# Performance work log

Hardware: AMD Instinct MI355X
Metric: run time of the kernel (lower is better)

Reference implementation:

```python
import jax, jax.numpy as jnp
import numpy as np

N = 50000
E = 1600000
IN_CH = 34
HID = 64
OUT = 64
NEG_SLOPE = 0.2


def _gat_layer(x, src, dst, W, a_src, a_dst, bias, heads, out_ch, concat):
    n = x.shape[0]
    xw = (x @ W).reshape(n, heads, out_ch)                      # [N,H,C]
    al_src = jnp.sum(xw * a_src[None], axis=-1)                  # [N,H]
    al_dst = jnp.sum(xw * a_dst[None], axis=-1)                  # [N,H]
    e = jax.nn.leaky_relu(al_src[src] + al_dst[dst], NEG_SLOPE)  # [E,H]
    # segment softmax over incoming edges of each dst node (self-loops ensure non-empty)
    m = jax.ops.segment_max(e, dst, num_segments=n)              # [N,H]
    ex = jnp.exp(e - m[dst])
    denom = jax.ops.segment_sum(ex, dst, num_segments=n)         # [N,H]
    alpha = ex / denom[dst]                                      # [E,H]
    msg = xw[src] * alpha[:, :, None]                            # [E,H,C]
    out = jax.ops.segment_sum(msg, dst, num_segments=n)          # [N,H,C]
    if concat:
        out = out.reshape(n, heads * out_ch)
    else:
        out = out.mean(axis=1)
    return out + bias


def setup_inputs() -> dict:
    key = jax.random.key(0)
    ks = jax.random.split(key, 12)
    x = jax.random.normal(ks[0], (N, IN_CH), dtype=jnp.float32)
    edge_index = jax.random.randint(ks[1], (2, E), 0, N, dtype=jnp.int64)
    # layer 1: heads=2, concat -> 128
    W1 = jax.random.normal(ks[2], (IN_CH, 2 * HID), dtype=jnp.float32) * 0.1
    a_src1 = jax.random.normal(ks[3], (2, HID), dtype=jnp.float32) * 0.1
    a_dst1 = jax.random.normal(ks[4], (2, HID), dtype=jnp.float32) * 0.1
    b1 = jnp.zeros((2 * HID,), dtype=jnp.float32)
    # layer 2: heads=1, mean
    W2 = jax.random.normal(ks[5], (2 * HID, OUT), dtype=jnp.float32) * 0.1
    a_src2 = jax.random.normal(ks[6], (1, OUT), dtype=jnp.float32) * 0.1
    a_dst2 = jax.random.normal(ks[7], (1, OUT), dtype=jnp.float32) * 0.1
    b2 = jnp.zeros((OUT,), dtype=jnp.float32)
    return {"x": x, "edge_index": edge_index, "W1": W1, "a_src1": a_src1,
            "a_dst1": a_dst1, "b1": b1, "W2": W2, "a_src2": a_src2,
            "a_dst2": a_dst2, "b2": b2}


def reference(x, edge_index, W1, a_src1, a_dst1, b1, W2, a_src2, a_dst2, b2):
    n = x.shape[0]
    loops = jnp.arange(n, dtype=edge_index.dtype)
    src = jnp.concatenate([edge_index[0], loops])  # PyG GATConv add_self_loops=True
    dst = jnp.concatenate([edge_index[1], loops])
    h = _gat_layer(x, src, dst, W1, a_src1, a_dst1, b1, heads=2, out_ch=HID, concat=True)
    h = jax.nn.relu(h)
    out = _gat_layer(h, src, dst, W2, a_src2, a_dst2, b2, heads=1, out_ch=OUT, concat=False)
    return out
```

## Files before the change

kernel.cpp:

```cpp
#include <hip/hip_runtime.h>
#include <math.h>

#define N_NODES 50000
#define E_EDGES 1600000
#define IN_CH   34
#define NEG     0.2f
#define NB      196
#define CAP     10000

typedef __attribute__((ext_vector_type(2))) float fv2;

static __device__ __forceinline__ unsigned short f2bf(float f) {
    unsigned int u = __float_as_uint(f);
    u += 0x7fffu + ((u >> 16) & 1u);
    return (unsigned short)(u >> 16);
}
static __device__ __forceinline__ float bflo(unsigned int u) {
    return __uint_as_float(u << 16);
}
static __device__ __forceinline__ float bfhi(unsigned int u) {
    return __uint_as_float(u & 0xffff0000u);
}
static __device__ __forceinline__ float lrelu_exp(float e) {
    return expf(e > 0.f ? e : NEG * e);
}

static __device__ __forceinline__ int scan256_excl(int v, int* wsum) {
    const int lane = threadIdx.x & 63, wv = threadIdx.x >> 6;
    int x = v;
    #pragma unroll
    for (int off = 1; off < 64; off <<= 1) {
        int y = __shfl_up(x, off);
        if (lane >= off) x += y;
    }
    if (lane == 63) wsum[wv] = x;
    __syncthreads();
    if (threadIdx.x < 4) {
        int s = wsum[threadIdx.x];
        #pragma unroll
        for (int off = 1; off < 4; off <<= 1) {
            int y = __shfl_up(s, off);
            if ((int)threadIdx.x >= off) s += y;
        }
        wsum[threadIdx.x] = s;
    }
    __syncthreads();
    const int woff = wv ? wsum[wv - 1] : 0;
    return woff + x - v;
}

__global__ __launch_bounds__(256) void k_bin_node1(
    const int* __restrict__ srcA, const int* __restrict__ dstA,
    int* __restrict__ gcur, unsigned int* __restrict__ binned,
    const float* __restrict__ x, const float* __restrict__ W1,
    const float* __restrict__ a_src, const float* __restrict__ a_dst,
    unsigned short* __restrict__ xw1b,
    float* __restrict__ al_s, float* __restrict__ al_d)
{
    __shared__ __align__(16) char sm[69664];
    const int tid = threadIdx.x;

    if (blockIdx.x < NB) {
        unsigned int* raw  = (unsigned int*)sm;
        unsigned int* ebuf = (unsigned int*)(sm + 32768);
        int* cnt  = (int*)(sm + 65536);
        int* loff = (int*)(sm + 66560);
        int* lcur = (int*)(sm + 67584);
        int* cur  = (int*)(sm + 68608);
        int* wsum = (int*)(sm + 69632);
        cnt[tid] = 0;
        __syncthreads();
        const int base = blockIdx.x * 8192;
        #pragma unroll
        for (int i = 0; i < 32; ++i) {
            const int e = base + i * 256 + tid;
            if (e < E_EDGES) {
                const int d = dstA[e], s = srcA[e];
                raw[i * 256 + tid] = ((unsigned int)d << 16) | (unsigned int)s;
                atomicAdd(&cnt[d >> 8], 1);
            }
        }
        __syncthreads();
        const int v = cnt[tid];
        const int excl = scan256_excl(v, wsum);
        loff[tid] = excl;
        lcur[tid] = excl;
        cur[tid] = (tid < NB && v > 0) ? (tid * CAP + atomicAdd(&gcur[tid], v)) : 0;
        __syncthreads();
        const int mE = min(8192, E_EDGES - base);
        #pragma unroll
        for (int i = 0; i < 32; ++i) {
            const int p = i * 256 + tid;
            if (p < mE) {
                const unsigned int u = raw[p];
                const int q = atomicAdd(&lcur[u >> 24], 1);
                ebuf[q] = u;
            }
        }
        __syncthreads();
        #pragma unroll
        for (int i = 0; i < 32; ++i) {
            const int p = i * 256 + tid;
            if (p < mE) {
                const unsigned int u = ebuf[p];
                const int b = (int)(u >> 24);
                binned[cur[b] + (p - loff[b])] = u;
            }
        }
    } else {
        float* sW  = (float*)sm;
        float* sx  = (float*)(sm + 17952);
        float* sas = (float*)(sm + 22432);
        float* sad = (float*)(sm + 22944);
        for (int i = tid; i < IN_CH * 128; i += 256) {
            int k = i >> 7, c = i & 127;
            sW[k * 132 + c] = W1[i];
        }
        if (tid < 128) { sas[tid] = a_src[tid]; sad[tid] = a_dst[tid]; }
        const int n0 = (blockIdx.x - NB) * 32;
        for (int i = tid; i < 32 * IN_CH; i += 256) {
            int n = i / IN_CH;
            sx[n * 35 + (i - n * IN_CH)] = (n0 + n < N_NODES) ? x[n0 * IN_CH + i] : 0.f;
        }
        __syncthreads();

        const int tc = tid & 31, tn = tid >> 5;
        float acc[4][4] = {{0.f}};
        for (int k = 0; k < IN_CH; ++k) {
            const float4 wv = *reinterpret_cast<const float4*>(&sW[k * 132 + 4 * tc]);
            #pragma unroll
            for (int j = 0; j < 4; ++j) {
                const float hj = sx[(4 * tn + j) * 35 + k];
                acc[j][0] += hj * wv.x; acc[j][1] += hj * wv.y;
                acc[j][2] += hj * wv.z; acc[j][3] += hj * wv.w;
            }
        }
        #pragma unroll
        for (int j = 0; j < 4; ++j) {
            const int node = n0 + 4 * tn + j;
            float ps = 0.f, pd = 0.f;
            #pragma unroll
            for (int c = 0; c < 4; ++c) {
                ps += acc[j][c] * sas[4 * tc + c];
                pd += acc[j][c] * sad[4 * tc + c];
            }
            #pragma unroll
            for (int off = 1; off < 16; off <<= 1) {
                ps += __shfl_xor(ps, off);
                pd += __shfl_xor(pd, off);
            }
            if (node < N_NODES) {
                if ((tc & 15) == 0) {
                    int h = tc >> 4;
                    al_s[node * 2 + h] = ps;
                    al_d[node * 2 + h] = pd;
                }
                ushort4 u;
                u.x = f2bf(acc[j][0]); u.y = f2bf(acc[j][1]);
                u.z = f2bf(acc[j][2]); u.w = f2bf(acc[j][3]);
                *reinterpret_cast<ushort4*>(&xw1b[node * 128 + 4 * tc]) = u;
            }
        }
    }
}

__global__ __launch_bounds__(256) void k_fine(
    const int* __restrict__ gcur, const unsigned int* __restrict__ binned,
    int2* __restrict__ rowspan, int* __restrict__ sorted_src)
{
    __shared__ unsigned int sbin[CAP];
    __shared__ int cnt[256], lcur[256];
    __shared__ int wsum[4];
    const int tid = threadIdx.x;
    const int b = blockIdx.x;
    const int bbase = b * CAP;
    const int cntb = gcur[b];
    cnt[tid] = 0;
    __syncthreads();
    for (int p = tid; p < cntb; p += 256) {
        const unsigned int u = binned[bbase + p];
        sbin[p] = u;
        atomicAdd(&cnt[(u >> 16) & 255], 1);
    }
    __syncthreads();
    const int v = cnt[tid];
    const int excl = scan256_excl(v, wsum);
    const int node = b * 256 + tid;
    if (node < N_NODES) rowspan[node] = make_int2(bbase + excl, bbase + excl + v);
    lcur[tid] = excl;
    __syncthreads();
    for (int p = tid; p < cntb; p += 256) {
        const unsigned int u = sbin[p];
        const int q = atomicAdd(&lcur[(u >> 16) & 255], 1);
        sorted_src[bbase + q] = (int)(u & 0xffffu);
    }
}

__global__ __launch_bounds__(256) void k_gather1(
    const int2* __restrict__ rowspan, const int* __restrict__ sorted_src,
    const unsigned int* __restrict__ xw1u,
    const float* __restrict__ al_s, const float* __restrict__ al_d,
    const float* __restrict__ b1, float* __restrict__ hbuf)
{
    __shared__ float4 AB[2][4][32];
    const int wave = threadIdx.x >> 6;
    const int lane = threadIdx.x & 63;
    const int node = (blockIdx.x * 256 + threadIdx.x) >> 6;
    if (node >= N_NODES) return;
    const int2 span = rowspan[node];
    const int head = lane >> 5;

    const float2 ald  = *reinterpret_cast<const float2*>(&al_d[node * 2]);
    const float2 als0 = *reinterpret_cast<const float2*>(&al_s[node * 2]);
    const float w0h0 = lrelu_exp(als0.x + ald.x);
    const float w0h1 = lrelu_exp(als0.y + ald.y);
    const float wself = head ? w0h1 : w0h0;

    const unsigned int su = xw1u[node * 64 + lane];
    fv2 accX = { wself * bflo(su), wself * bfhi(su) };
    fv2 accY = { 0.f, 0.f };
    float dv0 = 0.f, dv1 = 0.f;
    const float4* ABh = AB[head][wave];

    for (int base = span.x; base < span.y; base += 64) {
        const int rem = span.y - base;
        const int m = rem < 64 ? rem : 64;
        const int mp = (m + 1) & ~1;
        if (lane < m) {
            const int s = sorted_src[base + lane];
            const float2 als = *reinterpret_cast<const float2*>(&al_s[s * 2]);
            const float w0 = lrelu_exp(als.x + ald.x);
            const float w1 = lrelu_exp(als.y + ald.y);
            dv0 += w0; dv1 += w1;
            const float offf = __int_as_float(s << 6);
            ((float2*)&AB[0][wave][lane >> 1])[lane & 1] = make_float2(offf, w0);
            ((float2*)&AB[1][wave][lane >> 1])[lane & 1] = make_float2(offf, w1);
        } else if (lane < mp) {
            const float offf = __int_as_float(node << 6);
            ((float2*)&AB[0][wave][lane >> 1])[lane & 1] = make_float2(offf, 0.f);
            ((float2*)&AB[1][wave][lane >> 1])[lane & 1] = make_float2(offf, 0.f);
        }
        const int P = mp >> 1;
        int p = 0;
        for (; p + 4 <= P; p += 4) {
            const float4 q0 = ABh[p + 0];
            const float4 q1 = ABh[p + 1];
            const float4 q2 = ABh[p + 2];
            const float4 q3 = ABh[p + 3];
            const unsigned int a0 = xw1u[__float_as_int(q0.x) + lane];
            const unsigned int b0 = xw1u[__float_as_int(q0.z) + lane];
            const unsigned int a1 = xw1u[__float_as_int(q1.x) + lane];
            const unsigned int b1v = xw1u[__float_as_int(q1.z) + lane];
            const unsigned int a2 = xw1u[__float_as_int(q2.x) + lane];
            const unsigned int b2 = xw1u[__float_as_int(q2.z) + lane];
            const unsigned int a3 = xw1u[__float_as_int(q3.x) + lane];
            const unsigned int b3 = xw1u[__float_as_int(q3.z) + lane];
            fv2 f;
            f.x = bflo(a0); f.y = bfhi(a0); accX += f * q0.y;
            f.x = bflo(b0); f.y = bfhi(b0); accY += f * q0.w;
            f.x = bflo(a1); f.y = bfhi(a1); accX += f * q1.y;
            f.x = bflo(b1v); f.y = bfhi(b1v); accY += f * q1.w;
            f.x = bflo(a2); f.y = bfhi(a2); accX += f * q2.y;
            f.x = bflo(b2); f.y = bfhi(b2); accY += f * q2.w;
            f.x = bflo(a3); f.y = bfhi(a3); accX += f * q3.y;
            f.x = bflo(b3); f.y = bfhi(b3); accY += f * q3.w;
        }
        for (; p < P; ++p) {
            const float4 q = ABh[p];
            const unsigned int a = xw1u[__float_as_int(q.x) + lane];
            const unsigned int b = xw1u[__float_as_int(q.z) + lane];
            fv2 f;
            f.x = bflo(a); f.y = bfhi(a); accX += f * q.y;
            f.x = bflo(b); f.y = bfhi(b); accY += f * q.w;
        }
    }
    accX += accY;
    #pragma unroll
    for (int off = 32; off; off >>= 1) {
        dv0 += __shfl_xor(dv0, off);
        dv1 += __shfl_xor(dv1, off);
    }
    const float den = head ? (dv1 + w0h1) : (dv0 + w0h0);
    const float2 bv = *reinterpret_cast<const float2*>(&b1[2 * lane]);
    float o0 = accX.x / den + bv.x;
    float o1 = accX.y / den + bv.y;
    o0 = o0 > 0.f ? o0 : 0.f;
    o1 = o1 > 0.f ? o1 : 0.f;
    *reinterpret_cast<float2*>(&hbuf[node * 128 + 2 * lane]) = make_float2(o0, o1);
}

__global__ __launch_bounds__(256) void k_node2(
    const float* __restrict__ hbuf, const float* __restrict__ W2,
    const float* __restrict__ a_src, const float* __restrict__ a_dst,
    unsigned short* __restrict__ xw2b, float* __restrict__ al_s, float* __restrict__ al_d)
{
    __shared__ float sW[128 * 64];
    __shared__ float sh[64 * 129];
    __shared__ float sas[64], sad[64];
    const int tid = threadIdx.x;
    for (int i = tid; i < 128 * 64; i += 256) sW[i] = W2[i];
    if (tid < 64) { sas[tid] = a_src[tid]; sad[tid] = a_dst[tid]; }
    const int n0 = blockIdx.x * 64;
    for (int i = tid; i < 64 * 128; i += 256) {
        int n = i >> 7, c = i & 127;
        sh[n * 129 + c] = (n0 + n < N_NODES) ? hbuf[(long)(n0 + n) * 128 + c] : 0.f;
    }
    __syncthreads();

    const int tc = tid & 15, tn = tid >> 4;
    float acc[4][4] = {{0.f}};
    for (int k = 0; k < 128; ++k) {
        const float4 wv = *reinterpret_cast<const float4*>(&sW[k * 64 + 4 * tc]);
        #pragma unroll
        for (int j = 0; j < 4; ++j) {
            const float hj = sh[(4 * tn + j) * 129 + k];
            acc[j][0] += hj * wv.x; acc[j][1] += hj * wv.y;
            acc[j][2] += hj * wv.z; acc[j][3] += hj * wv.w;
        }
    }
    #pragma unroll
    for (int j = 0; j < 4; ++j) {
        const int node = n0 + 4 * tn + j;
        float ps = 0.f, pd = 0.f;
        #pragma unroll
        for (int c = 0; c < 4; ++c) {
            ps += acc[j][c] * sas[4 * tc + c];
            pd += acc[j][c] * sad[4 * tc + c];
        }
        #pragma unroll
        for (int off = 1; off < 16; off <<= 1) {
            ps += __shfl_xor(ps, off);
            pd += __shfl_xor(pd, off);
        }
        if (node < N_NODES) {
            if (tc == 0) { al_s[node] = ps; al_d[node] = pd; }
            ushort4 u;
            u.x = f2bf(acc[j][0]); u.y = f2bf(acc[j][1]);
            u.z = f2bf(acc[j][2]); u.w = f2bf(acc[j][3]);
            *reinterpret_cast<ushort4*>(&xw2b[node * 64 + 4 * tc]) = u;
        }
    }
}

__global__ __launch_bounds__(256) void k_gather2(
    const int2* __restrict__ rowspan, const int* __restrict__ sorted_src,
    const unsigned int* __restrict__ xw2u,
    const float* __restrict__ al_s, const float* __restrict__ al_d,
    const float* __restrict__ b2, float* __restrict__ out)
{
    __shared__ float4 AB[4][32];
    const int wave = threadIdx.x >> 6;
    const int lane = threadIdx.x & 63;
    const int node = (blockIdx.x * 256 + threadIdx.x) >> 6;
    if (node >= N_NODES) return;
    const int2 span = rowspan[node];
    const int li = lane & 31, hsel = lane >> 5;

    const float ald = al_d[node];
    const float w0s = lrelu_exp(al_s[node] + ald);
    const unsigned int su = xw2u[node * 32 + li];
    const float wself = hsel ? 0.f : w0s;
    fv2 acc = { wself * bflo(su), wself * bfhi(su) };
    float dv = 0.f;
    const float4* ABw = AB[wave];

    for (int base = span.x; base < span.y; base += 64) {
        const int rem = span.y - base;
        const int m = rem < 64 ? rem : 64;
        const int mp = (m + 3) & ~3;
        if (lane < m) {
            const int s = sorted_src[base + lane];
            const float w = lrelu_exp(al_s[s] + ald);
            dv += w;
            ((float2*)&AB[wave][lane >> 1])[lane & 1] =
                make_float2(__int_as_float(s << 5), w);
        } else if (lane < mp) {
            ((float2*)&AB[wave][lane >> 1])[lane & 1] =
                make_float2(__int_as_float(node << 5), 0.f);
        }
        const int P = mp >> 1;
        int p = hsel;
        for (; p + 2 < P; p += 4) {
            const float4 qA = ABw[p];
            const float4 qB = ABw[p + 2];
            const unsigned int aA = xw2u[__float_as_int(qA.x) + li];
            const unsigned int bA = xw2u[__float_as_int(qA.z) + li];
            const unsigned int aB = xw2u[__float_as_int(qB.x) + li];
            const unsigned int bB = xw2u[__float_as_int(qB.z) + li];
            fv2 f;
            f.x = bflo(aA); f.y = bfhi(aA); acc += f * qA.y;
            f.x = bflo(bA); f.y = bfhi(bA); acc += f * qA.w;
            f.x = bflo(aB); f.y = bfhi(aB); acc += f * qB.y;
            f.x = bflo(bB); f.y = bfhi(bB); acc += f * qB.w;
        }
        for (; p < P; p += 2) {
            const float4 q = ABw[p];
            const unsigned int a = xw2u[__float_as_int(q.x) + li];
            const unsigned int b = xw2u[__float_as_int(q.z) + li];
            fv2 f;
            f.x = bflo(a); f.y = bfhi(a); acc += f * q.y;
            f.x = bflo(b); f.y = bfhi(b); acc += f * q.w;
        }
    }
    acc.x += __shfl_xor(acc.x, 32);
    acc.y += __shfl_xor(acc.y, 32);
    #pragma unroll
    for (int off = 32; off; off >>= 1) dv += __shfl_xor(dv, off);
    if (lane < 32) {
        const float den = dv + w0s;
        const float2 bv = *reinterpret_cast<const float2*>(&b2[2 * li]);
        *reinterpret_cast<float2*>(&out[node * 64 + 2 * li]) =
            make_float2(acc.x / den + bv.x, acc.y / den + bv.y);
    }
}

extern "C" void kernel_launch(void* const* d_in, const int* in_sizes, int n_in,
                              void* d_out, int out_size, void* d_ws, size_t ws_size,
                              hipStream_t stream)
{
    const float* x   = (const float*)d_in[0];
    const int*   ei  = (const int*)d_in[1];
    const float* W1  = (const float*)d_in[2];
    const float* as1 = (const float*)d_in[3];
    const float* ad1 = (const float*)d_in[4];
    const float* b1  = (const float*)d_in[5];
    const float* W2  = (const float*)d_in[6];
    const float* as2 = (const float*)d_in[7];
    const float* ad2 = (const float*)d_in[8];
    const float* b2  = (const float*)d_in[9];
    float* out = (float*)d_out;

    const int* srcA = ei;
    const int* dstA = ei + E_EDGES;

    char* ws = (char*)d_ws;
    int2*  rowspan    = (int2*)(ws);
    int*   sorted_src = (int*)(ws + 409600);
    int*   gcur       = (int*)(ws + 8249600);
    float* al_s1      = (float*)(ws + 8251648);
    float* al_d1      = (float*)(ws + 8651648);
    float* al_s2      = (float*)(ws + 9051648);
    float* al_d2      = (float*)(ws + 9251648);
    unsigned short* xw1b = (unsigned short*)(ws + 9451648);
    float* hbuf       = (float*)(ws + 22251648);
    unsigned int* binned = (unsigned int*)hbuf;
    unsigned short* xw2b = (unsigned short*)(ws + 47851648);

    hipMemsetAsync(gcur, 0, NB * sizeof(int), stream);
    hipLaunchKernelGGL(k_bin_node1, dim3(NB + (N_NODES + 31) / 32), dim3(256), 0, stream,
                       srcA, dstA, gcur, binned,
                       x, W1, as1, ad1, xw1b, al_s1, al_d1);
    hipLaunchKernelGGL(k_fine, dim3(NB), dim3(256), 0, stream,
                       gcur, binned, rowspan, sorted_src);
    hipLaunchKernelGGL(k_gather1, dim3((N_NODES + 3) / 4), dim3(256), 0, stream,
                       rowspan, sorted_src, (const unsigned int*)xw1b,
                       al_s1, al_d1, b1, hbuf);
    hipLaunchKernelGGL(k_node2, dim3((N_NODES + 63) / 64), dim3(256), 0, stream,
                       hbuf, W2, as2, ad2, xw2b, al_s2, al_d2);
    hipLaunchKernelGGL(k_gather2, dim3((N_NODES + 3) / 4), dim3(256), 0, stream,
                       rowspan, sorted_src, (const unsigned int*)xw2b,
                       al_s2, al_d2, b2, out);
}
```

Measured before the change: 269.4 us.

## Use 1024-thread blocks for binning and fine sort, drop raw edge staging buffer

Raises the block size of the binning/node-projection kernel and the fine-sort kernel from 256 to 1024 threads. The binning path no longer stages packed edges in shared memory; it reads dst with int4 loads twice, once to count and again with src to scatter. This roughly halves LDS per block so more work fits per CU, and the node branch now handles 128 nodes per block. The costs are re-reading the edge arrays from global memory and leaving three quarters of the threads idle during the 256-wide scan.

```diff
diff --git a/kernel.cpp b/kernel.cpp
--- a/kernel.cpp
+++ b/kernel.cpp
@@ -25,7 +25,7 @@
     return expf(e > 0.f ? e : NEG * e);
 }
 
-static __device__ __forceinline__ int scan256_excl(int v, int* wsum) {
+static __device__ __forceinline__ int scan256_1024(int v, int* wsum) {
     const int lane = threadIdx.x & 63, wv = threadIdx.x >> 6;
     int x = v;
     #pragma unroll
@@ -33,7 +33,7 @@
         int y = __shfl_up(x, off);
         if (lane >= off) x += y;
     }
-    if (lane == 63) wsum[wv] = x;
+    if (wv < 4 && lane == 63) wsum[wv] = x;
     __syncthreads();
     if (threadIdx.x < 4) {
         int s = wsum[threadIdx.x];
@@ -45,11 +45,11 @@
         wsum[threadIdx.x] = s;
     }
     __syncthreads();
-    const int woff = wv ? wsum[wv - 1] : 0;
+    const int woff = (wv >= 1 && wv < 4) ? wsum[wv - 1] : 0;
     return woff + x - v;
 }
 
-__global__ __launch_bounds__(256) void k_bin_node1(
+__global__ __launch_bounds__(1024) void k_bin_node1(
     const int* __restrict__ srcA, const int* __restrict__ dstA,
     int* __restrict__ gcur, unsigned int* __restrict__ binned,
     const float* __restrict__ x, const float* __restrict__ W1,
@@ -57,68 +57,61 @@
     unsigned short* __restrict__ xw1b,
     float* __restrict__ al_s, float* __restrict__ al_d)
 {
-    __shared__ __align__(16) char sm[69664];
+    __shared__ __align__(16) char sm[36944];
     const int tid = threadIdx.x;
 
     if (blockIdx.x < NB) {
-        unsigned int* raw  = (unsigned int*)sm;
-        unsigned int* ebuf = (unsigned int*)(sm + 32768);
-        int* cnt  = (int*)(sm + 65536);
-        int* loff = (int*)(sm + 66560);
-        int* lcur = (int*)(sm + 67584);
-        int* cur  = (int*)(sm + 68608);
-        int* wsum = (int*)(sm + 69632);
-        cnt[tid] = 0;
+        unsigned int* ebuf = (unsigned int*)sm;
+        int* cnt  = (int*)(sm + 32768);
+        int* loff = (int*)(sm + 33792);
+        int* lcur = (int*)(sm + 34816);
+        int* cur  = (int*)(sm + 35840);
+        int* wsum = (int*)(sm + 36864);
+        if (tid < 256) cnt[tid] = 0;
         __syncthreads();
         const int base = blockIdx.x * 8192;
-        #pragma unroll
-        for (int i = 0; i < 32; ++i) {
-            const int e = base + i * 256 + tid;
-            if (e < E_EDGES) {
-                const int d = dstA[e], s = srcA[e];
-                raw[i * 256 + tid] = ((unsigned int)d << 16) | (unsigned int)s;
-                atomicAdd(&cnt[d >> 8], 1);
-            }
+        const int mE = min(8192, E_EDGES - base);
+        const int nq = mE >> 2;
+        for (int q = tid; q < nq; q += 1024) {
+            const int4 d4 = ((const int4*)(dstA + base))[q];
+            atomicAdd(&cnt[d4.x >> 8], 1);
+            atomicAdd(&cnt[d4.y >> 8], 1);
+            atomicAdd(&cnt[d4.z >> 8], 1);
+            atomicAdd(&cnt[d4.w >> 8], 1);
         }
         __syncthreads();
-        const int v = cnt[tid];
-        const int excl = scan256_excl(v, wsum);
-        loff[tid] = excl;
-        lcur[tid] = excl;
-        cur[tid] = (tid < NB && v > 0) ? (tid * CAP + atomicAdd(&gcur[tid], v)) : 0;
+        const int v = (tid < 256) ? cnt[tid] : 0;
+        const int excl = scan256_1024(v, wsum);
+        if (tid < 256) { loff[tid] = excl; lcur[tid] = excl; }
+        if (tid < NB) cur[tid] = (v > 0) ? (tid * CAP + atomicAdd(&gcur[tid], v)) : 0;
         __syncthreads();
-        const int mE = min(8192, E_EDGES - base);
-        #pragma unroll
-        for (int i = 0; i < 32; ++i) {
-            const int p = i * 256 + tid;
-            if (p < mE) {
-                const unsigned int u = raw[p];
-                const int q = atomicAdd(&lcur[u >> 24], 1);
-                ebuf[q] = u;
-            }
+        for (int q = tid; q < nq; q += 1024) {
+            const int4 d4 = ((const int4*)(dstA + base))[q];
+            const int4 s4 = ((const int4*)(srcA + base))[q];
+            int p;
+            p = atomicAdd(&lcur[d4.x >> 8], 1); ebuf[p] = ((unsigned)d4.x << 16) | (unsigned)s4.x;
+            p = atomicAdd(&lcur[d4.y >> 8], 1); ebuf[p] = ((unsigned)d4.y << 16) | (unsigned)s4.y;
+            p = atomicAdd(&lcur[d4.z >> 8], 1); ebuf[p] = ((unsigned)d4.z << 16) | (unsigned)s4.z;
+            p = atomicAdd(&lcur[d4.w >> 8], 1); ebuf[p] = ((unsigned)d4.w << 16) | (unsigned)s4.w;
         }
         __syncthreads();
-        #pragma unroll
-        for (int i = 0; i < 32; ++i) {
-            const int p = i * 256 + tid;
-            if (p < mE) {
-                const unsigned int u = ebuf[p];
-                const int b = (int)(u >> 24);
-                binned[cur[b] + (p - loff[b])] = u;
-            }
+        for (int p = tid; p < mE; p += 1024) {
+            const unsigned int u = ebuf[p];
+            const int b = (int)(u >> 24);
+            binned[cur[b] + (p - loff[b])] = u;
         }
     } else {
         float* sW  = (float*)sm;
         float* sx  = (float*)(sm + 17952);
-        float* sas = (float*)(sm + 22432);
-        float* sad = (float*)(sm + 22944);
-        for (int i = tid; i < IN_CH * 128; i += 256) {
+        float* sas = (float*)(sm + 35872);
+        float* sad = (float*)(sm + 36384);
+        for (int i = tid; i < IN_CH * 128; i += 1024) {
             int k = i >> 7, c = i & 127;
             sW[k * 132 + c] = W1[i];
         }
         if (tid < 128) { sas[tid] = a_src[tid]; sad[tid] = a_dst[tid]; }
-        const int n0 = (blockIdx.x - NB) * 32;
-        for (int i = tid; i < 32 * IN_CH; i += 256) {
+        const int n0 = (blockIdx.x - NB) * 128;
+        for (int i = tid; i < 128 * IN_CH; i += 1024) {
             int n = i / IN_CH;
             sx[n * 35 + (i - n * IN_CH)] = (n0 + n < N_NODES) ? x[n0 * IN_CH + i] : 0.f;
         }
@@ -164,7 +157,7 @@
     }
 }
 
-__global__ __launch_bounds__(256) void k_fine(
+__global__ __launch_bounds__(1024) void k_fine(
     const int* __restrict__ gcur, const unsigned int* __restrict__ binned,
     int2* __restrict__ rowspan, int* __restrict__ sorted_src)
 {
@@ -175,21 +168,23 @@
     const int b = blockIdx.x;
     const int bbase = b * CAP;
     const int cntb = gcur[b];
-    cnt[tid] = 0;
-    __syncthreads();
-    for (int p = tid; p < cntb; p += 256) {
+    if (tid < 256) cnt[tid] = 0;
+    __syncthreads();
+    for (int p = tid; p < cntb; p += 1024) {
         const unsigned int u = binned[bbase + p];
         sbin[p] = u;
         atomicAdd(&cnt[(u >> 16) & 255], 1);
     }
     __syncthreads();
-    const int v = cnt[tid];
-    const int excl = scan256_excl(v, wsum);
-    const int node = b * 256 + tid;
-    if (node < N_NODES) rowspan[node] = make_int2(bbase + excl, bbase + excl + v);
-    lcur[tid] = excl;
-    __syncthreads();
-    for (int p = tid; p < cntb; p += 256) {
+    const int v = (tid < 256) ? cnt[tid] : 0;
+    const int excl = scan256_1024(v, wsum);
+    if (tid < 256) {
+        lcur[tid] = excl;
+        const int node = b * 256 + tid;
+        if (node < N_NODES) rowspan[node] = make_int2(bbase + excl, bbase + excl + v);
+    }
+    __syncthreads();
+    for (int p = tid; p < cntb; p += 1024) {
         const unsigned int u = sbin[p];
         const int q = atomicAdd(&lcur[(u >> 16) & 255], 1);
         sorted_src[bbase + q] = (int)(u & 0xffffu);
@@ -447,10 +442,10 @@
     unsigned short* xw2b = (unsigned short*)(ws + 47851648);
 
     hipMemsetAsync(gcur, 0, NB * sizeof(int), stream);
-    hipLaunchKernelGGL(k_bin_node1, dim3(NB + (N_NODES + 31) / 32), dim3(256), 0, stream,
+    hipLaunchKernelGGL(k_bin_node1, dim3(NB + (N_NODES + 127) / 128), dim3(1024), 0, stream,
                        srcA, dstA, gcur, binned,
                        x, W1, as1, ad1, xw1b, al_s1, al_d1);
-    hipLaunchKernelGGL(k_fine, dim3(NB), dim3(256), 0, stream,
+    hipLaunchKernelGGL(k_fine, dim3(NB), dim3(1024), 0, stream,
                        gcur, binned, rowspan, sorted_src);
     hipLaunchKernelGGL(k_gather1, dim3((N_NODES + 3) / 4), dim3(256), 0, stream,
                        rowspan, sorted_src, (const unsigned int*)xw1b,
```

After: 350.4 us. 30.1% more time.
